# Performance work log

Hardware: AMD Instinct MI355X
Metric: run time of the kernel (lower is better)

The kernel has to match this reference:

```python
import jax, jax.numpy as jnp
import numpy as np

D_MODEL, D_MLP, D_HEAD, N_HEADS, SEQ, BATCH = 1024, 4096, 64, 16, 2048, 2


def setup_inputs() -> dict:
    key = jax.random.key(0)
    ks = jax.random.split(key, 7)
    s = 1.0 / np.sqrt(D_MODEL)
    return {
        "x": jax.random.normal(ks[0], (BATCH, SEQ, D_MODEL), jnp.float32),
        "W_K": jax.random.normal(ks[1], (N_HEADS, D_HEAD, D_MODEL), jnp.float32) * s,
        "W_Q": jax.random.normal(ks[2], (N_HEADS, D_HEAD, D_MODEL), jnp.float32) * s,
        "W_V": jax.random.normal(ks[3], (N_HEADS, D_HEAD, D_MODEL), jnp.float32) * s,
        "W_O": jax.random.normal(ks[4], (D_MODEL, N_HEADS * D_HEAD), jnp.float32) * s,
        "W_in": jax.random.normal(ks[5], (D_MLP, D_MODEL), jnp.float32) * s,
        "b_in": jnp.zeros((D_MLP,), jnp.float32),
        "W_out": jax.random.normal(ks[6], (D_MODEL, D_MLP), jnp.float32) * s,
        "b_out": jnp.zeros((D_MODEL,), jnp.float32),
    }


def _block(x, W_K, W_Q, W_V, W_O, W_in, b_in, W_out, b_out):
    S = x.shape[-2]
    # attention
    k = jnp.einsum('ihd,bpd->biph', W_K, x)
    q = jnp.einsum('ihd,bpd->biph', W_Q, x)
    v = jnp.einsum('ihd,bpd->biph', W_V, x)
    scores = jnp.einsum('biph,biqh->biqp', k, q)  # [B,H,S(query q),S(key p)]
    causal = jnp.tril(jnp.ones((S, S), x.dtype))
    masked = jnp.tril(scores) - 1e10 * (1.0 - causal)
    attn = jax.nn.softmax(masked / np.sqrt(D_HEAD), axis=-1)
    z = jnp.einsum('biph,biqp->biqh', v, attn)  # [B,H,S,d_head]
    z_flat = jnp.transpose(z, (0, 2, 1, 3)).reshape(x.shape[0], S, -1)  # b q (i h)
    attn_out = jnp.einsum('df,bqf->bqd', W_O, z_flat)
    x = x + attn_out
    # MLP
    h = jax.nn.relu(jnp.einsum('md,bpd->bpm', W_in, x) + b_in)
    x = x + jnp.einsum('dm,bpm->bpd', W_out, h) + b_out
    return x


def reference(x, W_K, W_Q, W_V, W_O, W_in, b_in, W_out, b_out):
    return _block(x, W_K, W_Q, W_V, W_O, W_in, b_in, W_out, b_out)
```

## Files before the change

### kernel.cpp

```cpp
#include <hip/hip_runtime.h>

typedef unsigned short u16;
typedef __bf16 bf16x8 __attribute__((ext_vector_type(8)));
typedef float f32x4 __attribute__((ext_vector_type(4)));
typedef u16 u16x8 __attribute__((ext_vector_type(8), may_alias));
typedef u16 u16x4 __attribute__((ext_vector_type(4), may_alias));
typedef unsigned int u32x4 __attribute__((ext_vector_type(4)));

#define D_MODEL 1024
#define D_MLP   4096
#define D_HEAD  64
#define N_HEADS 16
#define SEQ     2048
#define BATCH   2
#define BS      (BATCH * SEQ)
#define QKV_N   3072
#define QSCALE  0.18033688011112042f

__device__ __forceinline__ u16 f2b(float f) {
  unsigned u = __builtin_bit_cast(unsigned, f);
  u += 0x7fffu + ((u >> 16) & 1u);
  return (u16)(u >> 16);
}

__device__ __forceinline__ unsigned cvtpk_bf16(float lo, float hi) {
  unsigned r;
  asm("v_cvt_pk_bf16_f32 %0, %1, %2" : "=v"(r) : "v"(lo), "v"(hi));
  return r;
}

__device__ __forceinline__ void gload_lds16(const u16* g, u16* l) {
  __builtin_amdgcn_global_load_lds(
      (const __attribute__((address_space(1))) unsigned int*)g,
      (__attribute__((address_space(3))) unsigned int*)l, 16, 0, 0);
}

__global__ __launch_bounds__(256) void cvt_kernel(const float* __restrict__ in,
                                                  u16* __restrict__ out, int n4) {
  int i = blockIdx.x * 256 + threadIdx.x;
  if (i >= n4) return;
  float4 v = ((const float4*)in)[i];
  u16x4 o;
  o[0] = f2b(v.x); o[1] = f2b(v.y); o[2] = f2b(v.z); o[3] = f2b(v.w);
  ((u16x4*)out)[i] = o;
}

template<int MODE>
__global__ __launch_bounds__(256) void gemm_bt(
    const u16* __restrict__ A, const u16* __restrict__ Bw,
    int M, int N, int K,
    u16* __restrict__ outb, float* __restrict__ outf,
    const float* __restrict__ resid, const float* __restrict__ bias,
    u16* __restrict__ vtp, int gx)
{
  __shared__ u16 Asm_[128 * 64];
  __shared__ u16 Bsm_[128 * 64];
  const int t = threadIdx.x;
  const int lane = t & 63;
  const int l15 = lane & 15, l4 = lane >> 4;
  const int w = t >> 6;
  const int wr = w >> 1, wc = w & 1;

  const int xcd = blockIdx.x & 7;
  const int local = blockIdx.x >> 3;
  const int rw = gx >> 2;
  const int rx = xcd & 3, ry = xcd >> 2;
  const int c = local >> 4, r0 = local & 15;
  int bx = rx * rw + c;
  const int by = ry * 16 + r0;
  int z = 0;
  if (MODE == 3) { z = bx >> 3; bx &= 7; }
  const int m0 = by * 128;
  const int n0 = bx * 128;
  const int kb = (MODE == 3) ? z * (K >> 1) : 0;
  const int ke = (MODE == 3) ? kb + (K >> 1) : K;

  f32x4 acc[4][4] = {};

  for (int k0 = kb; k0 < ke; k0 += 64) {
    __syncthreads();
#pragma unroll
    for (int i = 0; i < 4; ++i) {
      int s = i * 256 + t;
      int row = s >> 3;
      int sl = s & 7;
      int gc = ((sl ^ (row & 7)) << 3);
      const u16* ga = A + (size_t)(m0 + row) * K + (k0 + gc);
      const u16* gb = Bw + (size_t)(n0 + row) * K + (k0 + gc);
      u16* la = Asm_ + (i * 256 + (t & ~63)) * 8;
      u16* lb = Bsm_ + (i * 256 + (t & ~63)) * 8;
      gload_lds16(ga, la);
      gload_lds16(gb, lb);
    }
    asm volatile("s_waitcnt vmcnt(0)" ::: "memory");
    __syncthreads();
#pragma unroll
    for (int kk = 0; kk < 2; ++kk) {
      bf16x8 af[4], bfr[4];
#pragma unroll
      for (int mi = 0; mi < 4; ++mi) {
        int row = wr * 64 + mi * 16 + l15;
        int sl2 = (kk * 4 + l4) ^ (row & 7);
        u16x8 ua = *(const u16x8*)(Asm_ + row * 64 + sl2 * 8);
        af[mi] = __builtin_bit_cast(bf16x8, ua);
      }
#pragma unroll
      for (int ni = 0; ni < 4; ++ni) {
        int row = wc * 64 + ni * 16 + l15;
        int sl2 = (kk * 4 + l4) ^ (row & 7);
        u16x8 ub = *(const u16x8*)(Bsm_ + row * 64 + sl2 * 8);
        bfr[ni] = __builtin_bit_cast(bf16x8, ub);
      }
#pragma unroll
      for (int mi = 0; mi < 4; ++mi)
#pragma unroll
        for (int ni = 0; ni < 4; ++ni)
          acc[mi][ni] = __builtin_amdgcn_mfma_f32_16x16x32_bf16(af[mi], bfr[ni], acc[mi][ni], 0, 0, 0);
    }
  }

#pragma unroll
  for (int mi = 0; mi < 4; ++mi) {
    int rowb = m0 + wr * 64 + mi * 16 + l4 * 4;
#pragma unroll
    for (int ni = 0; ni < 4; ++ni) {
      int col = n0 + wc * 64 + ni * 16 + l15;
#pragma unroll
      for (int r = 0; r < 4; ++r) {
        float v = acc[mi][ni][r];
        int row = rowb + r;
        if (MODE == 0) {
          if (col < 2048) {
            float o = (col < 1024) ? v * QSCALE : v;
            outb[((size_t)row << 11) + col] = f2b(o);
          } else {
            int c2 = col - 2048;
            size_t vi = (((size_t)((row >> 11) * 1024 + c2)) << 11) + (row & (SEQ - 1));
            vtp[vi] = f2b(v);
          }
        } else if (MODE == 3) {
          outf[(size_t)z * M * N + (size_t)row * N + col] = v;
        } else {
          size_t idx = (size_t)row * N + col;
          if (MODE == 1) {
            float o = v + resid[idx];
            outf[idx] = o;
            outb[idx] = f2b(o);
          } else {
            float o = v + bias[col];
            o = o > 0.f ? o : 0.f;
            outb[idx] = f2b(o);
          }
        }
      }
    }
  }
}

__global__ __launch_bounds__(256) void reduce2_kernel(const float* __restrict__ part,
                                                      const float* __restrict__ resid,
                                                      const float* __restrict__ bias,
                                                      float* __restrict__ out) {
  const int i = blockIdx.x * 256 + threadIdx.x;
  float4 a = ((const float4*)part)[i];
  float4 b = ((const float4*)(part + (size_t)BS * D_MODEL))[i];
  float4 r = ((const float4*)resid)[i];
  float4 bi = ((const float4*)bias)[i & 255];
  float4 o;
  o.x = a.x + b.x + r.x + bi.x;
  o.y = a.y + b.y + r.y + bi.y;
  o.z = a.z + b.z + r.z + bi.z;
  o.w = a.w + b.w + r.w + bi.w;
  ((float4*)out)[i] = o;
}

__global__ __launch_bounds__(256) void attn_kernel(const u16* __restrict__ qk,
                                                   const u16* __restrict__ vT,
                                                   u16* __restrict__ zb)
{
  __shared__ u16 Kl[2][32 * 64];
  __shared__ u16 Vl[2][64 * 40];
  const int t = threadIdx.x;
  const int w = t >> 6;
  const int lane = t & 63;
  const int l15 = lane & 15, l4 = lane >> 4;
  const int blk = blockIdx.x;
  const int bh = blk & 31;
  const int qb = 15 - (blk >> 5);
  const int b = bh >> 4, h = bh & 15;
  const int q0w = qb * 128 + w * 32;
  const int myLast = 4 * qb + w;
  const int ptmax = 4 * qb + 3;

  bf16x8 qf[2][2];
#pragma unroll
  for (int s = 0; s < 2; ++s) {
    const u16* qp = qk + (((size_t)(b * SEQ + q0w + s * 16 + l15)) << 11) + h * 64 + l4 * 8;
    qf[s][0] = __builtin_bit_cast(bf16x8, *(const u16x8*)(qp));
    qf[s][1] = __builtin_bit_cast(bf16x8, *(const u16x8*)(qp + 32));
  }

  const int srow = t >> 3;
  const int sgc = ((t & 7) ^ (srow & 7)) * 8;
  const u16* kgbase = qk + (((size_t)(b * SEQ + srow)) << 11) + 1024 + h * 64 + sgc;
  u16* kldst = &Kl[0][0] + (t & ~63) * 8;
  const int vd = t >> 2, vch = (t & 3) * 8;
  const u16* vgbase = vT + (((size_t)(bh * 64 + vd)) << 11) + vch;

  f32x4 zacc[2][4] = {};
  float m_run[2] = {-1e30f, -1e30f}, l_run[2] = {0.f, 0.f};

  auto compute = [&](int buf, int pt) {
    bf16x8 kf[2][2];
#pragma unroll
    for (int ks = 0; ks < 2; ++ks) {
      int row = ks * 16 + l15;
#pragma unroll
      for (int kc = 0; kc < 2; ++kc) {
        int slot = (kc * 4 + l4) ^ (row & 7);
        kf[ks][kc] = __builtin_bit_cast(bf16x8, *(const u16x8*)&Kl[buf][row * 64 + slot * 8]);
      }
    }
    bf16x8 vf[2][4];
#pragma unroll
    for (int ks = 0; ks < 2; ++ks)
#pragma unroll
      for (int dn = 0; dn < 4; ++dn) {
        u16x4 v4 = *(const u16x4*)&Vl[buf][(dn * 16 + l15) * 40 + ks * 16 + l4 * 4];
        u16x8 v8 = __builtin_shufflevector(v4, v4, 0, 1, 2, 3, 0, 1, 2, 3);
        vf[ks][dn] = __builtin_bit_cast(bf16x8, v8);
      }

    const bool diag = (pt == myLast);
#pragma unroll
    for (int s = 0; s < 2; ++s) {
      f32x4 s0 = {}, s1 = {};
      __builtin_amdgcn_s_setprio(1);
      s0 = __builtin_amdgcn_mfma_f32_16x16x32_bf16(kf[0][0], qf[s][0], s0, 0, 0, 0);
      s0 = __builtin_amdgcn_mfma_f32_16x16x32_bf16(kf[0][1], qf[s][1], s0, 0, 0, 0);
      s1 = __builtin_amdgcn_mfma_f32_16x16x32_bf16(kf[1][0], qf[s][0], s1, 0, 0, 0);
      s1 = __builtin_amdgcn_mfma_f32_16x16x32_bf16(kf[1][1], qf[s][1], s1, 0, 0, 0);
      __builtin_amdgcn_s_setprio(0);

      if (diag) {
#pragma unroll
        for (int r = 0; r < 4; ++r) {
          const bool keep = (l4 * 4 + r <= l15);
          if (s == 0) {
            s0[r] = keep ? s0[r] : -1e30f;
            s1[r] = -1e30f;
          } else {
            s1[r] = keep ? s1[r] : -1e30f;
          }
        }
      }

      float mt = fmaxf(fmaxf(fmaxf(s0[0], s0[1]), fmaxf(s0[2], s0[3])),
                       fmaxf(fmaxf(s1[0], s1[1]), fmaxf(s1[2], s1[3])));
      mt = fmaxf(mt, __shfl_xor(mt, 16));
      mt = fmaxf(mt, __shfl_xor(mt, 32));
      const float mn = fmaxf(m_run[s], mt);
      const float sc = __builtin_amdgcn_exp2f(m_run[s] - mn);
      m_run[s] = mn;
      float p0v[4], p1v[4];
      float rs = 0.f;
#pragma unroll
      for (int r = 0; r < 4; ++r) {
        p0v[r] = __builtin_amdgcn_exp2f(s0[r] - mn);
        p1v[r] = __builtin_amdgcn_exp2f(s1[r] - mn);
        rs += p0v[r] + p1v[r];
      }
      rs += __shfl_xor(rs, 16);
      rs += __shfl_xor(rs, 32);
      l_run[s] = l_run[s] * sc + rs;

#pragma unroll
      for (int dn = 0; dn < 4; ++dn)
#pragma unroll
        for (int r = 0; r < 4; ++r) zacc[s][dn][r] *= sc;

      u32x4 pu0, pu1;
      pu0[0] = cvtpk_bf16(p0v[0], p0v[1]);
      pu0[1] = cvtpk_bf16(p0v[2], p0v[3]);
      pu0[2] = 0u; pu0[3] = 0u;
      pu1[0] = cvtpk_bf16(p1v[0], p1v[1]);
      pu1[1] = cvtpk_bf16(p1v[2], p1v[3]);
      pu1[2] = 0u; pu1[3] = 0u;
      const bf16x8 pa0 = __builtin_bit_cast(bf16x8, pu0);
      const bf16x8 pa1 = __builtin_bit_cast(bf16x8, pu1);

      __builtin_amdgcn_s_setprio(1);
#pragma unroll
      for (int dn = 0; dn < 4; ++dn) {
        zacc[s][dn] = __builtin_amdgcn_mfma_f32_16x16x32_bf16(vf[0][dn], pa0, zacc[s][dn], 0, 0, 0);
        zacc[s][dn] = __builtin_amdgcn_mfma_f32_16x16x32_bf16(vf[1][dn], pa1, zacc[s][dn], 0, 0, 0);
      }
      __builtin_amdgcn_s_setprio(0);
    }
  };

  gload_lds16(kgbase, kldst);
  {
    u16x8 v0 = *(const u16x8*)(vgbase);
    *(u16x8*)&Vl[0][vd * 40 + vch] = v0;
  }
  asm volatile("s_waitcnt vmcnt(0)" ::: "memory");
  __syncthreads();

  int cur = 0;
  for (int pt = 0; pt <= ptmax; ++pt) {
    const bool more = pt < ptmax;
    u16x8 vnext;
    if (more) {
      gload_lds16(kgbase + ((size_t)(pt + 1) << 16), kldst + (cur ^ 1) * (32 * 64));
      vnext = *(const u16x8*)(vgbase + (pt + 1) * 32);
    }
    if (pt <= myLast) compute(cur, pt);
    if (more) *(u16x8*)&Vl[cur ^ 1][vd * 40 + vch] = vnext;
    asm volatile("s_waitcnt vmcnt(0)" ::: "memory");
    __syncthreads();
    cur ^= 1;
  }

#pragma unroll
  for (int s = 0; s < 2; ++s) {
    const float inv = 1.f / l_run[s];
    const size_t rowoff = ((size_t)(b * SEQ + q0w + s * 16 + l15)) * D_MODEL + h * 64 + l4 * 4;
#pragma unroll
    for (int dn = 0; dn < 4; ++dn) {
      u16x4 o;
#pragma unroll
      for (int r = 0; r < 4; ++r) o[r] = f2b(zacc[s][dn][r] * inv);
      *(u16x4*)(zb + rowoff + dn * 16) = o;
    }
  }
}

extern "C" void kernel_launch(void* const* d_in, const int* in_sizes, int n_in,
                              void* d_out, int out_size, void* d_ws, size_t ws_size,
                              hipStream_t stream) {
  const float* x     = (const float*)d_in[0];
  const float* W_K   = (const float*)d_in[1];
  const float* W_Q   = (const float*)d_in[2];
  const float* W_V   = (const float*)d_in[3];
  const float* W_O   = (const float*)d_in[4];
  const float* W_in  = (const float*)d_in[5];
  const float* b_in  = (const float*)d_in[6];
  const float* W_out = (const float*)d_in[7];
  const float* b_out = (const float*)d_in[8];
  float* out = (float*)d_out;

  char* p = (char*)d_ws;
  u16* xb    = (u16*)p;            p += (size_t)BS * D_MODEL * 2;
  u16* wqkv  = (u16*)p;            p += (size_t)QKV_N * D_MODEL * 2;
  u16* wo_b  = (u16*)p;            p += (size_t)D_MODEL * D_MODEL * 2;
  u16* win_b = (u16*)p;            p += (size_t)D_MLP * D_MODEL * 2;
  u16* wout_b= (u16*)p;            p += (size_t)D_MODEL * D_MLP * 2;
  float* x1f = (float*)p;          p += (size_t)BS * D_MODEL * 4;
  u16* hb    = (u16*)p;            p += (size_t)BS * D_MLP * 2;
  u16* qk    = (u16*)p;            p += (size_t)BS * 2048 * 2;
  u16* vt    = (u16*)p;            p += (size_t)BATCH * 1024 * SEQ * 2;
  u16* zb    = (u16*)p;            p += (size_t)BS * D_MODEL * 2;
  u16* x1b   = (u16*)p;            p += (size_t)BS * D_MODEL * 2;
  float* part = (float*)qk;

  auto cvt = [&](const float* src, u16* dst, int n) {
    int n4 = n / 4;
    cvt_kernel<<<(n4 + 255) / 256, 256, 0, stream>>>(src, dst, n4);
  };
  cvt(x, xb, BS * D_MODEL);
  cvt(W_Q, wqkv + 0,                  N_HEADS * D_HEAD * D_MODEL);
  cvt(W_K, wqkv + 1024 * 1024,        N_HEADS * D_HEAD * D_MODEL);
  cvt(W_V, wqkv + 2 * 1024 * 1024,    N_HEADS * D_HEAD * D_MODEL);
  cvt(W_O, wo_b,  D_MODEL * D_MODEL);
  cvt(W_in, win_b, D_MLP * D_MODEL);
  cvt(W_out, wout_b, D_MODEL * D_MLP);

  gemm_bt<0><<<dim3(24 * 32), 256, 0, stream>>>(
      xb, wqkv, BS, QKV_N, D_MODEL, qk, nullptr, nullptr, nullptr, vt, 24);

  attn_kernel<<<dim3(512), 256, 0, stream>>>(qk, vt, zb);

  gemm_bt<1><<<dim3(8 * 32), 256, 0, stream>>>(
      zb, wo_b, BS, D_MODEL, D_MODEL, x1b, x1f, x, nullptr, nullptr, 8);

  gemm_bt<2><<<dim3(32 * 32), 256, 0, stream>>>(
      x1b, win_b, BS, D_MLP, D_MODEL, hb, nullptr, nullptr, b_in, nullptr, 32);

  gemm_bt<3><<<dim3(16 * 32), 256, 0, stream>>>(
      hb, wout_b, BS, D_MODEL, D_MLP, nullptr, part, nullptr, nullptr, nullptr, 16);

  reduce2_kernel<<<dim3(BS * D_MODEL / 4 / 256), 256, 0, stream>>>(part, x1f, b_out, out);
}
```

Before: 294.8 us.

## Double attention key tile to 64 and use full-width PV MFMA operands

The attention kernel now processes 64 keys per iteration instead of 32, which halves the number of barrier-synchronised loop steps. The P operand of the PV MFMA now fills all 8 bf16 slots instead of zero-padding half of them, so V is loaded from LDS as a full 8-element vector in a re-permuted layout. This cuts MFMA count per key and sync overhead. The cost is more LDS and registers, plus extra masked work on the diagonal tile for waves whose last 32-key block falls mid-tile.

```diff
diff --git a/kernel.cpp b/kernel.cpp
--- a/kernel.cpp
+++ b/kernel.cpp
@@ -178,8 +178,8 @@
                                                    const u16* __restrict__ vT,
                                                    u16* __restrict__ zb)
 {
-  __shared__ u16 Kl[2][32 * 64];
-  __shared__ u16 Vl[2][64 * 40];
+  __shared__ u16 Kl[2][64 * 64];
+  __shared__ u16 Vl[2][64 * 72];
   const int t = threadIdx.x;
   const int w = t >> 6;
   const int lane = t & 63;
@@ -189,8 +189,8 @@
   const int qb = 15 - (blk >> 5);
   const int b = bh >> 4, h = bh & 15;
   const int q0w = qb * 128 + w * 32;
-  const int myLast = 4 * qb + w;
-  const int ptmax = 4 * qb + 3;
+  const int myLastT = (4 * qb + w) >> 1;
+  const int ttmaxB = 2 * qb + 1;
 
   bf16x8 qf[2][2];
 #pragma unroll
@@ -204,16 +204,16 @@
   const int sgc = ((t & 7) ^ (srow & 7)) * 8;
   const u16* kgbase = qk + (((size_t)(b * SEQ + srow)) << 11) + 1024 + h * 64 + sgc;
   u16* kldst = &Kl[0][0] + (t & ~63) * 8;
-  const int vd = t >> 2, vch = (t & 3) * 8;
-  const u16* vgbase = vT + (((size_t)(bh * 64 + vd)) << 11) + vch;
+  const int vd2 = t >> 2, q4 = t & 3;
+  const u16* vgbase = vT + (((size_t)(bh * 64 + vd2)) << 11);
 
   f32x4 zacc[2][4] = {};
   float m_run[2] = {-1e30f, -1e30f}, l_run[2] = {0.f, 0.f};
 
-  auto compute = [&](int buf, int pt) {
-    bf16x8 kf[2][2];
-#pragma unroll
-    for (int ks = 0; ks < 2; ++ks) {
+  auto compute = [&](int buf, int tt) {
+    bf16x8 kf[4][2];
+#pragma unroll
+    for (int ks = 0; ks < 4; ++ks) {
       int row = ks * 16 + l15;
 #pragma unroll
       for (int kc = 0; kc < 2; ++kc) {
@@ -223,53 +223,53 @@
     }
     bf16x8 vf[2][4];
 #pragma unroll
-    for (int ks = 0; ks < 2; ++ks)
-#pragma unroll
-      for (int dn = 0; dn < 4; ++dn) {
-        u16x4 v4 = *(const u16x4*)&Vl[buf][(dn * 16 + l15) * 40 + ks * 16 + l4 * 4];
-        u16x8 v8 = __builtin_shufflevector(v4, v4, 0, 1, 2, 3, 0, 1, 2, 3);
-        vf[ks][dn] = __builtin_bit_cast(bf16x8, v8);
-      }
-
-    const bool diag = (pt == myLast);
+    for (int g = 0; g < 2; ++g)
+#pragma unroll
+      for (int dn = 0; dn < 4; ++dn)
+        vf[g][dn] = __builtin_bit_cast(bf16x8,
+            *(const u16x8*)&Vl[buf][(dn * 16 + l15) * 72 + g * 32 + l4 * 8]);
+
+    const bool last = (tt == myLastT);
 #pragma unroll
     for (int s = 0; s < 2; ++s) {
-      f32x4 s0 = {}, s1 = {};
+      f32x4 sf[4] = {};
       __builtin_amdgcn_s_setprio(1);
-      s0 = __builtin_amdgcn_mfma_f32_16x16x32_bf16(kf[0][0], qf[s][0], s0, 0, 0, 0);
-      s0 = __builtin_amdgcn_mfma_f32_16x16x32_bf16(kf[0][1], qf[s][1], s0, 0, 0, 0);
-      s1 = __builtin_amdgcn_mfma_f32_16x16x32_bf16(kf[1][0], qf[s][0], s1, 0, 0, 0);
-      s1 = __builtin_amdgcn_mfma_f32_16x16x32_bf16(kf[1][1], qf[s][1], s1, 0, 0, 0);
+#pragma unroll
+      for (int ks = 0; ks < 4; ++ks) {
+        sf[ks] = __builtin_amdgcn_mfma_f32_16x16x32_bf16(kf[ks][0], qf[s][0], sf[ks], 0, 0, 0);
+        sf[ks] = __builtin_amdgcn_mfma_f32_16x16x32_bf16(kf[ks][1], qf[s][1], sf[ks], 0, 0, 0);
+      }
       __builtin_amdgcn_s_setprio(0);
 
-      if (diag) {
-#pragma unroll
-        for (int r = 0; r < 4; ++r) {
-          const bool keep = (l4 * 4 + r <= l15);
-          if (s == 0) {
-            s0[r] = keep ? s0[r] : -1e30f;
-            s1[r] = -1e30f;
-          } else {
-            s1[r] = keep ? s1[r] : -1e30f;
-          }
-        }
-      }
-
-      float mt = fmaxf(fmaxf(fmaxf(s0[0], s0[1]), fmaxf(s0[2], s0[3])),
-                       fmaxf(fmaxf(s1[0], s1[1]), fmaxf(s1[2], s1[3])));
+      if (last) {
+        const int qq = q0w + s * 16 + l15;
+        const int pb = tt * 64 + l4 * 4;
+#pragma unroll
+        for (int ks = 0; ks < 4; ++ks)
+#pragma unroll
+          for (int r = 0; r < 4; ++r)
+            sf[ks][r] = (pb + ks * 16 + r <= qq) ? sf[ks][r] : -1e30f;
+      }
+
+      float mk[4];
+#pragma unroll
+      for (int ks = 0; ks < 4; ++ks)
+        mk[ks] = fmaxf(fmaxf(sf[ks][0], sf[ks][1]), fmaxf(sf[ks][2], sf[ks][3]));
+      float mt = fmaxf(fmaxf(mk[0], mk[1]), fmaxf(mk[2], mk[3]));
       mt = fmaxf(mt, __shfl_xor(mt, 16));
       mt = fmaxf(mt, __shfl_xor(mt, 32));
       const float mn = fmaxf(m_run[s], mt);
       const float sc = __builtin_amdgcn_exp2f(m_run[s] - mn);
       m_run[s] = mn;
-      float p0v[4], p1v[4];
+      float pv[4][4];
       float rs = 0.f;
 #pragma unroll
-      for (int r = 0; r < 4; ++r) {
-        p0v[r] = __builtin_amdgcn_exp2f(s0[r] - mn);
-        p1v[r] = __builtin_amdgcn_exp2f(s1[r] - mn);
-        rs += p0v[r] + p1v[r];
-      }
+      for (int ks = 0; ks < 4; ++ks)
+#pragma unroll
+        for (int r = 0; r < 4; ++r) {
+          pv[ks][r] = __builtin_amdgcn_exp2f(sf[ks][r] - mn);
+          rs += pv[ks][r];
+        }
       rs += __shfl_xor(rs, 16);
       rs += __shfl_xor(rs, 32);
       l_run[s] = l_run[s] * sc + rs;
@@ -279,44 +279,65 @@
 #pragma unroll
         for (int r = 0; r < 4; ++r) zacc[s][dn][r] *= sc;
 
-      u32x4 pu0, pu1;
-      pu0[0] = cvtpk_bf16(p0v[0], p0v[1]);
-      pu0[1] = cvtpk_bf16(p0v[2], p0v[3]);
-      pu0[2] = 0u; pu0[3] = 0u;
-      pu1[0] = cvtpk_bf16(p1v[0], p1v[1]);
-      pu1[1] = cvtpk_bf16(p1v[2], p1v[3]);
-      pu1[2] = 0u; pu1[3] = 0u;
-      const bf16x8 pa0 = __builtin_bit_cast(bf16x8, pu0);
-      const bf16x8 pa1 = __builtin_bit_cast(bf16x8, pu1);
+      bf16x8 pa[2];
+#pragma unroll
+      for (int g = 0; g < 2; ++g) {
+        u32x4 pu;
+        pu[0] = cvtpk_bf16(pv[2 * g][0], pv[2 * g][1]);
+        pu[1] = cvtpk_bf16(pv[2 * g][2], pv[2 * g][3]);
+        pu[2] = cvtpk_bf16(pv[2 * g + 1][0], pv[2 * g + 1][1]);
+        pu[3] = cvtpk_bf16(pv[2 * g + 1][2], pv[2 * g + 1][3]);
+        pa[g] = __builtin_bit_cast(bf16x8, pu);
+      }
 
       __builtin_amdgcn_s_setprio(1);
 #pragma unroll
       for (int dn = 0; dn < 4; ++dn) {
-        zacc[s][dn] = __builtin_amdgcn_mfma_f32_16x16x32_bf16(vf[0][dn], pa0, zacc[s][dn], 0, 0, 0);
-        zacc[s][dn] = __builtin_amdgcn_mfma_f32_16x16x32_bf16(vf[1][dn], pa1, zacc[s][dn], 0, 0, 0);
+        zacc[s][dn] = __builtin_amdgcn_mfma_f32_16x16x32_bf16(vf[0][dn], pa[0], zacc[s][dn], 0, 0, 0);
+        zacc[s][dn] = __builtin_amdgcn_mfma_f32_16x16x32_bf16(vf[1][dn], pa[1], zacc[s][dn], 0, 0, 0);
       }
       __builtin_amdgcn_s_setprio(0);
     }
   };
 
   gload_lds16(kgbase, kldst);
+  gload_lds16(kgbase + ((size_t)1 << 16), kldst + 2048);
   {
-    u16x8 v0 = *(const u16x8*)(vgbase);
-    *(u16x8*)&Vl[0][vd * 40 + vch] = v0;
+    const u16* vg = vgbase;
+    u16x4 a0 = *(const u16x4*)(vg + q4 * 4);
+    u16x4 a1 = *(const u16x4*)(vg + 16 + q4 * 4);
+    u16x4 b0 = *(const u16x4*)(vg + 32 + q4 * 4);
+    u16x4 b1 = *(const u16x4*)(vg + 48 + q4 * 4);
+    *(u16x8*)&Vl[0][vd2 * 72 + q4 * 8] =
+        __builtin_shufflevector(a0, a1, 0, 1, 2, 3, 4, 5, 6, 7);
+    *(u16x8*)&Vl[0][vd2 * 72 + 32 + q4 * 8] =
+        __builtin_shufflevector(b0, b1, 0, 1, 2, 3, 4, 5, 6, 7);
   }
   asm volatile("s_waitcnt vmcnt(0)" ::: "memory");
   __syncthreads();
 
   int cur = 0;
-  for (int pt = 0; pt <= ptmax; ++pt) {
-    const bool more = pt < ptmax;
-    u16x8 vnext;
+  for (int tt = 0; tt <= ttmaxB; ++tt) {
+    const bool more = tt < ttmaxB;
+    u16x4 a0, a1, b0, b1;
     if (more) {
-      gload_lds16(kgbase + ((size_t)(pt + 1) << 16), kldst + (cur ^ 1) * (32 * 64));
-      vnext = *(const u16x8*)(vgbase + (pt + 1) * 32);
-    }
-    if (pt <= myLast) compute(cur, pt);
-    if (more) *(u16x8*)&Vl[cur ^ 1][vd * 40 + vch] = vnext;
+      const u16* kg = kgbase + ((size_t)(tt + 1) << 17);
+      u16* kld = kldst + (cur ^ 1) * 4096;
+      gload_lds16(kg, kld);
+      gload_lds16(kg + ((size_t)1 << 16), kld + 2048);
+      const u16* vg = vgbase + (tt + 1) * 64;
+      a0 = *(const u16x4*)(vg + q4 * 4);
+      a1 = *(const u16x4*)(vg + 16 + q4 * 4);
+      b0 = *(const u16x4*)(vg + 32 + q4 * 4);
+      b1 = *(const u16x4*)(vg + 48 + q4 * 4);
+    }
+    if (tt <= myLastT) compute(cur, tt);
+    if (more) {
+      *(u16x8*)&Vl[cur ^ 1][vd2 * 72 + q4 * 8] =
+          __builtin_shufflevector(a0, a1, 0, 1, 2, 3, 4, 5, 6, 7);
+      *(u16x8*)&Vl[cur ^ 1][vd2 * 72 + 32 + q4 * 8] =
+          __builtin_shufflevector(b0, b1, 0, 1, 2, 3, 4, 5, 6, 7);
+    }
     asm volatile("s_waitcnt vmcnt(0)" ::: "memory");
     __syncthreads();
     cur ^= 1;
```

After: 269.1 us. -8.7%, faster.
